# Kernel optimization log

Measured on AMD Instinct MI355X. Metric: run time of the kernel, lower is better.

Reference implementation:

```python
import jax, jax.numpy as jnp
import numpy as np

N = 8192          # pre-NMS proposals per image
NUM_CLASSES = 80  # COCO


def setup_inputs() -> dict:
    key = jax.random.key(0)
    k1, k2, k3, k4 = jax.random.split(key, 4)
    # valid x1y1x2y2 boxes on a ~1000px canvas with side lengths in [1, 201]
    xy = jax.random.uniform(k1, (N, 2), dtype=jnp.float32) * 1000.0
    wh = jax.random.uniform(k2, (N, 2), dtype=jnp.float32) * 200.0 + 1.0
    boxes = jnp.concatenate([xy, xy + wh], axis=1)          # [N, 4]
    scores = jax.random.uniform(k3, (N,), dtype=jnp.float32)
    labels = jax.random.randint(k4, (N,), 0, NUM_CLASSES, dtype=jnp.int32)
    return {
        "boxes": boxes,
        "scores": scores,
        "labels": labels,
        "thresh": jnp.float32(0.5),
        "max_proposals": 0,  # 0 => keep all survivors (matches torch default)
    }


def _iou_matrix(b):
    """Pairwise IoU of [N,4] x1y1x2y2 boxes -> [N,N]."""
    area = (b[:, 2] - b[:, 0]) * (b[:, 3] - b[:, 1])        # [N]
    lt = jnp.maximum(b[:, None, :2], b[None, :, :2])        # [N,N,2]
    rb = jnp.minimum(b[:, None, 2:], b[None, :, 2:])        # [N,N,2]
    wh = jnp.clip(rb - lt, 0.0)
    inter = wh[..., 0] * wh[..., 1]                         # [N,N]
    return inter / (area[:, None] + area[None, :] - inter)


def reference(boxes, scores, labels, thresh, max_proposals):
    """Multi-label greedy NMS.

    Suppresses a lower-scoring box iff IoU > thresh AND same label.
    Returns (kept_boxes_sorted_by_score_with_suppressed_zeroed [N,4],
             order [N]  original indices in descending-score order,
             keep  [N]  bool mask over the sorted order).
    torch's `boxes[keep], keep` is the masked gather of these (dynamic
    shape, so we return the static-shape masked form).
    """
    n = boxes.shape[0]
    order = jnp.argsort(-scores)                            # descending score
    b = boxes[order]                                        # [N,4] sorted
    l = labels[order]                                       # [N]
    iou = _iou_matrix(b)                                    # [N,N]
    idx = jnp.arange(n)
    # j can be suppressed by i only if i ranks higher (i < j)
    sup = (iou > thresh) & (l[:, None] == l[None, :]) & (idx[None, :] > idx[:, None])

    def body(i, keep):
        # if box i survives, kill everything it suppresses
        return jnp.where(keep[i], keep & ~sup[i], keep)

    keep = jax.lax.fori_loop(0, n, body, jnp.ones(n, dtype=bool))

    if max_proposals > 0:  # static Python int
        keep = keep & (jnp.cumsum(keep.astype(jnp.int32)) <= max_proposals)

    kept_boxes = jnp.where(keep[:, None], b, 0.0)           # [N,4]
    return kept_boxes, order.astype(jnp.int32), keep
```

## Files before the change

kernel.cpp:

```cpp
#include <hip/hip_runtime.h>
#include <stdint.h>


#define NUM_CLASSES 80
#define MROW 256

typedef unsigned long long u64;
typedef unsigned int u32;
typedef unsigned short u16;

__device__ __forceinline__ u32 mono_key(float s) {
    u32 u = __float_as_uint(s);
    return (u & 0x80000000u) ? ~u : (u | 0x80000000u);
}
__device__ __forceinline__ u64 make_key(float s, int j) {
    return ((u64)mono_key(s) << 32) | (u32)(~j);
}
__device__ __forceinline__ u64 rdlane64(u64 v, int l) {
    u32 lo = (u32)__builtin_amdgcn_readlane((int)(u32)v, l);
    u32 hi = (u32)__builtin_amdgcn_readlane((int)(u32)(v >> 32), l);
    return ((u64)hi << 32) | lo;
}

__global__ void __launch_bounds__(256)
rank_kernel(const float* __restrict__ scores, u16* __restrict__ rank16,
            int* __restrict__ done, int N) {
    __shared__ u64 ks[512];
    const int t = threadIdx.x;
    if (blockIdx.x == 0 && blockIdx.y == 0 && t == 0) *done = 0;
    const int j0 = blockIdx.y * 512;
    for (int q = t; q < 512; q += 256) {
        int j = j0 + q;
        ks[q] = (j < N) ? make_key(scores[j], j) : 0ULL;
    }
    __syncthreads();
    const int i0 = blockIdx.x * 512 + t;
    const int i1 = i0 + 256;
    const u64 k0 = (i0 < N) ? make_key(scores[i0], i0) : ~0ULL;
    const u64 k1 = (i1 < N) ? make_key(scores[i1], i1) : ~0ULL;
    int c0 = 0, c1 = 0;
    #pragma unroll 16
    for (int q = 0; q < 512; ++q) {
        u64 k = ks[q];
        c0 += (k > k0) ? 1 : 0;
        c1 += (k > k1) ? 1 : 0;
    }
    if (i0 < N) rank16[blockIdx.y * N + i0] = (u16)c0;
    if (i1 < N) rank16[blockIdx.y * N + i1] = (u16)c1;
}

__global__ void __launch_bounds__(512)
nms2_kernel(const float* __restrict__ boxes, const int* __restrict__ labels,
            const u16* __restrict__ rank16, const float* __restrict__ thresh_p,
            const int* __restrict__ mp_ptr, int* __restrict__ done,
            float* __restrict__ out_boxes, float* __restrict__ out_order,
            float* __restrict__ out_keep, int N, int nseg) {
    const int c    = blockIdx.x;
    const int t    = threadIdx.x;
    const int lane = t & 63;
    const int w    = t >> 6;
    const float th = *thresh_p;
    const int   mp = *mp_ptr;
    const float4* b4 = (const float4*)boxes;

    __shared__ float4 lbox[MROW];
    __shared__ int    rrs[MROW];
    __shared__ u64    R[MROW][4];
    __shared__ int    ilist[MROW];
    __shared__ u32    rs[MROW];
    __shared__ u64    aliveS[4];
    __shared__ int    m_s;

    if (t == 0) m_s = 0;
    if (t < MROW) rs[t] = 0;
    ((u64*)R)[t]       = 0ULL;
    ((u64*)R)[t + 512] = 0ULL;
    __syncthreads();

    const int4* lab4 = (const int4*)labels;
    for (int base = 0; base < N; base += 2048) {
        int i0 = base + t * 4;
        if (i0 < N) {
            int4 lv = lab4[(base >> 2) + t];
            #pragma unroll
            for (int k = 0; k < 4; ++k) {
                int lab = (k == 0) ? lv.x : (k == 1) ? lv.y : (k == 2) ? lv.z : lv.w;
                if (lab == c) {
                    int i = i0 + k;
                    int pos = atomicAdd(&m_s, 1);
                    if (pos < MROW) {
                        ilist[pos] = i;
                    } else {
                        u32 s = 0;
                        for (int g = 0; g < nseg; ++g) s += rank16[g * N + i];
                        ((float4*)out_boxes)[s] = b4[i];
                        out_keep[s]  = 1.0f;
                        out_order[s] = (float)i;
                    }
                }
            }
        }
    }
    __syncthreads();
    const int mtot = m_s;
    const int me   = (mtot < MROW) ? mtot : MROW;

    if (me > 0) {
        for (int u = t; u < me * 16; u += 512) {
            int e = u >> 4;
            int g = u & 15;
            atomicAdd(&rs[e], (u32)rank16[g * N + ilist[e]]);
        }
        __syncthreads();

        for (int e = t; e < me; e += 512) {
            u32 r = rs[e];
            int cr = 0;
            for (int e2 = 0; e2 < me; ++e2) cr += (rs[e2] < r) ? 1 : 0;
            int i = ilist[e];
            out_order[r] = (float)i;
            lbox[cr] = b4[i];
            rrs[cr]  = (int)r;
        }
        __syncthreads();

        for (int sw = 0; sw * 64 < me; ++sw) {
            const int myslot = sw * 64 + lane;
            float4 mb = make_float4(0.f, 0.f, 0.f, 0.f);
            float mar = 0.f;
            if (myslot < me) { mb = lbox[myslot]; mar = (mb.z - mb.x) * (mb.w - mb.y); }
            int lim = (sw + 1) * 64; if (lim > me) lim = me;
            int chunk = (lim + 7) >> 3;
            int lo = w * chunk;
            int hi = lo + chunk; if (hi > lim) hi = lim;
            for (int i = lo; i < hi; ++i) {
                float4 bi = lbox[i];
                float ai = (bi.z - bi.x) * (bi.w - bi.y);
                float lx = fmaxf(bi.x, mb.x), ly = fmaxf(bi.y, mb.y);
                float rx = fminf(bi.z, mb.z), ry = fminf(bi.w, mb.w);
                float ww = fmaxf(rx - lx, 0.f), hh = fmaxf(ry - ly, 0.f);
                float inter = ww * hh;
                float iou = inter / (ai + mar - inter);
                u64 mask = __ballot(iou > th && myslot > i);
                if (lane == 0 && mask) R[i][sw] = mask;
            }
        }
        __syncthreads();

        if (w == 0) {
            u64 a0 = 0, a1 = 0, a2 = 0, a3 = 0;
            {
                u64 rw0 = R[lane][0];
                u64 nz0 = __ballot(rw0 != 0ULL);
                int n = me > 64 ? 64 : me;
                u64 a = (n >= 64) ? ~0ULL : ((1ULL << n) - 1ULL);
                for (int bb = 0; bb < n; ++bb)
                    if (((a & nz0) >> bb) & 1ULL) a &= ~rdlane64(rw0, bb);
                a0 = a;
            }
            if (me > 64) {
                u64 rw0 = R[lane][1], rw1 = R[64 + lane][1];
                u64 nz0 = __ballot(rw0 != 0ULL), nz1 = __ballot(rw1 != 0ULL);
                int n = (me - 64) > 64 ? 64 : (me - 64);
                u64 a = (n >= 64) ? ~0ULL : ((1ULL << n) - 1ULL);
                for (int bb = 0; bb < 64; ++bb)
                    if (((a0 & nz0) >> bb) & 1ULL) a &= ~rdlane64(rw0, bb);
                for (int bb = 0; bb < n; ++bb)
                    if (((a & nz1) >> bb) & 1ULL) a &= ~rdlane64(rw1, bb);
                a1 = a;
            }
            if (me > 128) {
                u64 rw0 = R[lane][2], rw1 = R[64 + lane][2], rw2 = R[128 + lane][2];
                u64 nz0 = __ballot(rw0 != 0ULL), nz1 = __ballot(rw1 != 0ULL),
                    nz2 = __ballot(rw2 != 0ULL);
                int n = (me - 128) > 64 ? 64 : (me - 128);
                u64 a = (n >= 64) ? ~0ULL : ((1ULL << n) - 1ULL);
                for (int bb = 0; bb < 64; ++bb)
                    if (((a0 & nz0) >> bb) & 1ULL) a &= ~rdlane64(rw0, bb);
                for (int bb = 0; bb < 64; ++bb)
                    if (((a1 & nz1) >> bb) & 1ULL) a &= ~rdlane64(rw1, bb);
                for (int bb = 0; bb < n; ++bb)
                    if (((a & nz2) >> bb) & 1ULL) a &= ~rdlane64(rw2, bb);
                a2 = a;
            }
            if (me > 192) {
                u64 rw0 = R[lane][3], rw1 = R[64 + lane][3],
                    rw2 = R[128 + lane][3], rw3 = R[192 + lane][3];
                u64 nz0 = __ballot(rw0 != 0ULL), nz1 = __ballot(rw1 != 0ULL),
                    nz2 = __ballot(rw2 != 0ULL), nz3 = __ballot(rw3 != 0ULL);
                int n = me - 192;
                u64 a = (n >= 64) ? ~0ULL : ((1ULL << n) - 1ULL);
                for (int bb = 0; bb < 64; ++bb)
                    if (((a0 & nz0) >> bb) & 1ULL) a &= ~rdlane64(rw0, bb);
                for (int bb = 0; bb < 64; ++bb)
                    if (((a1 & nz1) >> bb) & 1ULL) a &= ~rdlane64(rw1, bb);
                for (int bb = 0; bb < 64; ++bb)
                    if (((a2 & nz2) >> bb) & 1ULL) a &= ~rdlane64(rw2, bb);
                for (int bb = 0; bb < n; ++bb)
                    if (((a & nz3) >> bb) & 1ULL) a &= ~rdlane64(rw3, bb);
                a3 = a;
            }
            if (lane < 4)
                aliveS[lane] = (lane == 0) ? a0 : (lane == 1) ? a1
                             : (lane == 2) ? a2 : a3;
        }
        __syncthreads();

        if (t < me) {
            int kept = (int)((aliveS[t >> 6] >> (t & 63)) & 1ULL);
            int r = rrs[t];
            float4 bbx = lbox[t];
            float4 z = make_float4(0.f, 0.f, 0.f, 0.f);
            ((float4*)out_boxes)[r] = kept ? bbx : z;
            out_keep[r] = kept ? 1.0f : 0.0f;
        }
    }

    if (mp > 0) {
        __syncthreads();
        __threadfence();
        if (t == 0) {
            int old = atomicAdd(done, 1);
            if (old == NUM_CLASSES - 1) {
                __threadfence();
                int cnt = 0;
                for (int j = 0; j < N; ++j) {
                    if (out_keep[j] > 0.0f) {
                        if (++cnt > mp) {
                            out_keep[j] = 0.0f;
                            ((float4*)out_boxes)[j] = make_float4(0.f, 0.f, 0.f, 0.f);
                        }
                    }
                }
            }
        }
    }
}

extern "C" void kernel_launch(void* const* d_in, const int* in_sizes, int n_in,
                              void* d_out, int out_size, void* d_ws, size_t ws_size,
                              hipStream_t stream) {
    const int N = in_sizes[0] / 4;
    const float* boxes  = (const float*)d_in[0];
    const float* scores = (const float*)d_in[1];
    const int*   labels = (const int*)d_in[2];
    const float* thresh = (const float*)d_in[3];
    const int*   maxp   = (const int*)d_in[4];

    float* out       = (float*)d_out;
    float* out_boxes = out;
    float* out_order = out + 4 * (size_t)N;
    float* out_keep  = out + 5 * (size_t)N;

    const int nseg = (N + 511) / 512;

    char* w = (char*)d_ws;
    int* done   = (int*)w;
    u16* rank16 = (u16*)(w + 64);

    const int gx = (N + 511) / 512;

    rank_kernel<<<dim3(gx, nseg), 256, 0, stream>>>(scores, rank16, done, N);
    nms2_kernel<<<NUM_CLASSES, 512, 0, stream>>>(boxes, labels, rank16, thresh,
                                                 maxp, done,
                                                 out_boxes, out_order, out_keep,
                                                 N, nseg);
}
```

Before: 30.99 us.

## Scatter sorted label keys once, then build per-class lists by ballot compaction

A new scatter kernel sums the per-segment ranks once per box, writes out_order, and stores a packed (index<<7 | label) key at each box's sorted position. Each per-class NMS block then has one wavefront scan the sorted keys with ballot/popcount, which yields an ordered member list without the per-class rank summation, atomics or O(m^2) in-block sort. The rank kernel also moves to 128 threads with four keys per thread. The cost is an extra kernel launch and extra workspace, and the hardcoded 16 segments plus 16-bit indices assume N of at most 8192.

```diff
diff --git a/kernel.cpp b/kernel.cpp
--- a/kernel.cpp
+++ b/kernel.cpp
@@ -22,39 +22,59 @@
     return ((u64)hi << 32) | lo;
 }
 
-__global__ void __launch_bounds__(256)
+__global__ void __launch_bounds__(128)
 rank_kernel(const float* __restrict__ scores, u16* __restrict__ rank16,
             int* __restrict__ done, int N) {
     __shared__ u64 ks[512];
     const int t = threadIdx.x;
     if (blockIdx.x == 0 && blockIdx.y == 0 && t == 0) *done = 0;
     const int j0 = blockIdx.y * 512;
-    for (int q = t; q < 512; q += 256) {
-        int j = j0 + q;
-        ks[q] = (j < N) ? make_key(scores[j], j) : 0ULL;
+    #pragma unroll
+    for (int p = 0; p < 4; ++p) {
+        int j = j0 + p * 128 + t;
+        ks[p * 128 + t] = (j < N) ? make_key(scores[j], j) : 0ULL;
     }
     __syncthreads();
     const int i0 = blockIdx.x * 512 + t;
-    const int i1 = i0 + 256;
+    const int i1 = i0 + 128, i2 = i0 + 256, i3 = i0 + 384;
     const u64 k0 = (i0 < N) ? make_key(scores[i0], i0) : ~0ULL;
     const u64 k1 = (i1 < N) ? make_key(scores[i1], i1) : ~0ULL;
-    int c0 = 0, c1 = 0;
-    #pragma unroll 16
+    const u64 k2 = (i2 < N) ? make_key(scores[i2], i2) : ~0ULL;
+    const u64 k3 = (i3 < N) ? make_key(scores[i3], i3) : ~0ULL;
+    int c0 = 0, c1 = 0, c2 = 0, c3 = 0;
+    #pragma unroll 8
     for (int q = 0; q < 512; ++q) {
         u64 k = ks[q];
         c0 += (k > k0) ? 1 : 0;
         c1 += (k > k1) ? 1 : 0;
-    }
-    if (i0 < N) rank16[blockIdx.y * N + i0] = (u16)c0;
-    if (i1 < N) rank16[blockIdx.y * N + i1] = (u16)c1;
+        c2 += (k > k2) ? 1 : 0;
+        c3 += (k > k3) ? 1 : 0;
+    }
+    u16* rp = rank16 + (size_t)blockIdx.y * N;
+    if (i0 < N) rp[i0] = (u16)c0;
+    if (i1 < N) rp[i1] = (u16)c1;
+    if (i2 < N) rp[i2] = (u16)c2;
+    if (i3 < N) rp[i3] = (u16)c3;
+}
+
+__global__ void __launch_bounds__(256)
+scat_kernel(const int* __restrict__ labels, const u16* __restrict__ rank16,
+            u32* __restrict__ skey, float* __restrict__ out_order, int N, int nseg) {
+    const int i = blockIdx.x * 256 + threadIdx.x;
+    if (i >= N) return;
+    u32 s = 0;
+    #pragma unroll
+    for (int g = 0; g < 16; ++g)
+        s += (u32)rank16[g * N + i];
+    out_order[s] = (float)i;
+    skey[s] = ((u32)i << 7) | (u32)labels[i];
 }
 
 __global__ void __launch_bounds__(512)
-nms2_kernel(const float* __restrict__ boxes, const int* __restrict__ labels,
-            const u16* __restrict__ rank16, const float* __restrict__ thresh_p,
-            const int* __restrict__ mp_ptr, int* __restrict__ done,
-            float* __restrict__ out_boxes, float* __restrict__ out_order,
-            float* __restrict__ out_keep, int N, int nseg) {
+nms3_kernel(const float* __restrict__ boxes, const u32* __restrict__ skey,
+            const float* __restrict__ thresh_p, const int* __restrict__ mp_ptr,
+            int* __restrict__ done,
+            float* __restrict__ out_boxes, float* __restrict__ out_keep, int N) {
     const int c    = blockIdx.x;
     const int t    = threadIdx.x;
     const int lane = t & 63;
@@ -64,64 +84,51 @@
     const float4* b4 = (const float4*)boxes;
 
     __shared__ float4 lbox[MROW];
-    __shared__ int    rrs[MROW];
+    __shared__ u16    il_i[MROW];
+    __shared__ u16    il_r[MROW];
     __shared__ u64    R[MROW][4];
-    __shared__ int    ilist[MROW];
-    __shared__ u32    rs[MROW];
     __shared__ u64    aliveS[4];
     __shared__ int    m_s;
 
-    if (t == 0) m_s = 0;
-    if (t < MROW) rs[t] = 0;
-    ((u64*)R)[t]       = 0ULL;
-    ((u64*)R)[t + 512] = 0ULL;
-    __syncthreads();
-
-    const int4* lab4 = (const int4*)labels;
-    for (int base = 0; base < N; base += 2048) {
-        int i0 = base + t * 4;
-        if (i0 < N) {
-            int4 lv = lab4[(base >> 2) + t];
+    if (w == 0) {
+        int running = 0;
+        for (int it = 0; it * 256 < N; ++it) {
+            const int base = it * 256;
+            u32 v0 = skey[base + lane];
+            u32 v1 = skey[base + 64 + lane];
+            u32 v2 = skey[base + 128 + lane];
+            u32 v3 = skey[base + 192 + lane];
             #pragma unroll
-            for (int k = 0; k < 4; ++k) {
-                int lab = (k == 0) ? lv.x : (k == 1) ? lv.y : (k == 2) ? lv.z : lv.w;
-                if (lab == c) {
-                    int i = i0 + k;
-                    int pos = atomicAdd(&m_s, 1);
+            for (int cb = 0; cb < 4; ++cb) {
+                u32 v = (cb == 0) ? v0 : (cb == 1) ? v1 : (cb == 2) ? v2 : v3;
+                bool hit = (v & 0x7Fu) == (u32)c;
+                u64 mask = __ballot(hit);
+                if (hit) {
+                    int pos = running + __popcll(mask & ((1ULL << lane) - 1ULL));
+                    int i = (int)(v >> 7);
+                    int r = base + cb * 64 + lane;
                     if (pos < MROW) {
-                        ilist[pos] = i;
+                        il_i[pos] = (u16)i;
+                        il_r[pos] = (u16)r;
                     } else {
-                        u32 s = 0;
-                        for (int g = 0; g < nseg; ++g) s += rank16[g * N + i];
-                        ((float4*)out_boxes)[s] = b4[i];
-                        out_keep[s]  = 1.0f;
-                        out_order[s] = (float)i;
+                        ((float4*)out_boxes)[r] = b4[i];
+                        out_keep[r] = 1.0f;
                     }
                 }
-            }
-        }
+                running += __popcll(mask);
+            }
+        }
+        if (lane == 0) m_s = running;
+    } else {
+        for (int q = t - 64; q < 1024; q += 448) ((u64*)R)[q] = 0ULL;
     }
     __syncthreads();
+
     const int mtot = m_s;
     const int me   = (mtot < MROW) ? mtot : MROW;
 
     if (me > 0) {
-        for (int u = t; u < me * 16; u += 512) {
-            int e = u >> 4;
-            int g = u & 15;
-            atomicAdd(&rs[e], (u32)rank16[g * N + ilist[e]]);
-        }
-        __syncthreads();
-
-        for (int e = t; e < me; e += 512) {
-            u32 r = rs[e];
-            int cr = 0;
-            for (int e2 = 0; e2 < me; ++e2) cr += (rs[e2] < r) ? 1 : 0;
-            int i = ilist[e];
-            out_order[r] = (float)i;
-            lbox[cr] = b4[i];
-            rrs[cr]  = (int)r;
-        }
+        if (t < me) lbox[t] = b4[il_i[t]];
         __syncthreads();
 
         for (int sw = 0; sw * 64 < me; ++sw) {
@@ -208,7 +215,7 @@
 
         if (t < me) {
             int kept = (int)((aliveS[t >> 6] >> (t & 63)) & 1ULL);
-            int r = rrs[t];
+            int r = (int)il_r[t];
             float4 bbx = lbox[t];
             float4 z = make_float4(0.f, 0.f, 0.f, 0.f);
             ((float4*)out_boxes)[r] = kept ? bbx : z;
@@ -257,12 +264,13 @@
     char* w = (char*)d_ws;
     int* done   = (int*)w;
     u16* rank16 = (u16*)(w + 64);
+    u32* skey   = (u32*)(w + 64 + (size_t)nseg * N * 2);
 
     const int gx = (N + 511) / 512;
 
-    rank_kernel<<<dim3(gx, nseg), 256, 0, stream>>>(scores, rank16, done, N);
-    nms2_kernel<<<NUM_CLASSES, 512, 0, stream>>>(boxes, labels, rank16, thresh,
-                                                 maxp, done,
-                                                 out_boxes, out_order, out_keep,
-                                                 N, nseg);
-}
+    rank_kernel<<<dim3(gx, nseg), 128, 0, stream>>>(scores, rank16, done, N);
+    scat_kernel<<<(N + 255) / 256, 256, 0, stream>>>(labels, rank16, skey,
+                                                     out_order, N, nseg);
+    nms3_kernel<<<NUM_CLASSES, 512, 0, stream>>>(boxes, skey, thresh, maxp, done,
+                                                 out_boxes, out_keep, N);
+}
```

New measurement: 47.11 us. 52.0% more time.
